# Kernel optimization log

Measured on AMD Instinct MI355X. Metric: run time of the kernel, lower is better.

The kernel has to match this reference:

```python
import jax, jax.numpy as jnp
import numpy as np
import math

D_MODEL = 1024
N_HEADS = 16
HEAD_DIM = 64


def setup_inputs() -> dict:
    key = jax.random.key(0)
    k_x, k_q, k_k, k_v, k_o = jax.random.split(key, 5)
    lecun = jax.nn.initializers.lecun_normal()
    return {
        "x": jax.random.normal(k_x, (4, 2048, D_MODEL), dtype=jnp.float32),
        "W_q": lecun(k_q, (N_HEADS, D_MODEL, HEAD_DIM), jnp.float32),
        "W_k": lecun(k_k, (N_HEADS, D_MODEL, HEAD_DIM), jnp.float32),
        "W_v": lecun(k_v, (N_HEADS, D_MODEL, HEAD_DIM), jnp.float32),
        "W_o": lecun(k_o, (D_MODEL, D_MODEL), jnp.float32),
    }


def reference(x, W_q, W_k, W_v, W_o):
    # x: [b, l, e]; W_{q,k,v}: [h, e, d]; W_o: [e, e]
    q = jnp.einsum('ble,hed->bhld', x, W_q)
    k = jnp.einsum('ble,hed->bhld', x, W_k)
    v = jnp.einsum('ble,hed->bhld', x, W_v)
    scores = jnp.einsum('bhld,bhsd->bhls', q, k) / math.sqrt(HEAD_DIM)
    attn = jax.nn.softmax(scores, axis=-1)
    av = jnp.einsum('bhls,bhsd->bhld', attn, v)  # [b, h, l, d]
    b, h, l, d = av.shape
    concat = jnp.transpose(av, (0, 2, 1, 3)).reshape(b, l, h * d)
    out = jnp.einsum('ble,eo->blo', concat, W_o)
    return jnp.asarray(out, dtype=jnp.float32)
```

## Files before the change

kernel.cpp:

```cpp
#include <hip/hip_runtime.h>

#define BATCH 4
#define LSEQ  2048
#define DM    1024
#define NH    16
#define HD    64
#define NTOK  (BATCH * LSEQ)

typedef _Float16 f16x8 __attribute__((ext_vector_type(8)));
typedef _Float16 f16x4 __attribute__((ext_vector_type(4)));
typedef __fp16   hf16x2 __attribute__((ext_vector_type(2)));
typedef float    f32x4 __attribute__((ext_vector_type(4)));

typedef __attribute__((address_space(1))) const unsigned int GU32;
typedef __attribute__((address_space(3))) unsigned int LU32;

__device__ __forceinline__ void gload_lds16(const _Float16* g, _Float16* l)
{
    __builtin_amdgcn_global_load_lds(
        (GU32*)(unsigned long long)g,
        (LU32*)(unsigned int)(unsigned long long)l, 16, 0, 0);
}


__global__ __launch_bounds__(256) void cvt_kernel(const float* __restrict__ src,
                                                  _Float16* __restrict__ dst, int n4)
{
    int i = blockIdx.x * 256 + threadIdx.x;
    if (i >= n4) return;
    float4 v = ((const float4*)src)[i];
    f16x4 h;
    h[0] = (_Float16)v.x; h[1] = (_Float16)v.y; h[2] = (_Float16)v.z; h[3] = (_Float16)v.w;
    ((f16x4*)dst)[i] = h;
}

__global__ __launch_bounds__(256) void tconv_kernel(const float* __restrict__ src,
                                                    _Float16* __restrict__ dst, int E, int D)
{
    const int d0 = blockIdx.x * 64, e0 = blockIdx.y * 64;
    const size_t mo = (size_t)blockIdx.z * E * D;
    src += mo; dst += mo;
    __shared__ float Ls[64][65];
    const int t = threadIdx.x;
    #pragma unroll
    for (int j = 0; j < 4; ++j) {
        int cidx = t + j * 256;
        int row = cidx >> 4, col4 = (cidx & 15) * 4;
        float4 v = *(const float4*)&src[(size_t)(e0 + row) * D + d0 + col4];
        Ls[row][col4] = v.x; Ls[row][col4+1] = v.y; Ls[row][col4+2] = v.z; Ls[row][col4+3] = v.w;
    }
    __syncthreads();
    const int dd = t & 63, sc = t >> 6;
    alignas(16) _Float16 tmp[16];
    #pragma unroll
    for (int i = 0; i < 16; ++i) tmp[i] = (_Float16)Ls[sc * 16 + i][dd];
    *(f16x8*)&dst[(size_t)(d0 + dd) * E + e0 + sc * 16]     = *(f16x8*)&tmp[0];
    *(f16x8*)&dst[(size_t)(d0 + dd) * E + e0 + sc * 16 + 8] = *(f16x8*)&tmp[8];
}

__global__ __launch_bounds__(256) void tv_kernel(const _Float16* __restrict__ v,
                                                 _Float16* __restrict__ vt)
{
    const int l0 = blockIdx.x * 64;
    const int bh = blockIdx.y;
    __shared__ _Float16 Ls[64][72];
    const int t = threadIdx.x;
    #pragma unroll
    for (int j = 0; j < 2; ++j) {
        int cidx = t + j * 256;
        int row = cidx >> 3, col8 = (cidx & 7) * 8;
        *(f16x8*)&Ls[row][col8] = *(const f16x8*)&v[((size_t)bh * LSEQ + l0 + row) * HD + col8];
    }
    __syncthreads();
    const int dd = t & 63, sc = t >> 6;
    alignas(16) _Float16 tmp[16];
    #pragma unroll
    for (int i = 0; i < 16; ++i) tmp[i] = Ls[sc * 16 + i][dd];
    *(f16x8*)&vt[((size_t)bh * HD + dd) * LSEQ + l0 + sc * 16]     = *(f16x8*)&tmp[0];
    *(f16x8*)&vt[((size_t)bh * HD + dd) * LSEQ + l0 + sc * 16 + 8] = *(f16x8*)&tmp[8];
}

template<int MODE>
__global__ __launch_bounds__(256) void gemm_kernel(
    const _Float16* __restrict__ A, const _Float16* __restrict__ B,
    float* __restrict__ out32,
    _Float16* __restrict__ qo, _Float16* __restrict__ ko, _Float16* __restrict__ vo)
{
    const int n0 = blockIdx.x * 128, m0 = blockIdx.y * 128;
    __shared__ _Float16 As[128 * 64];
    __shared__ _Float16 Bs[128 * 64];
    const int t = threadIdx.x;
    const int lane = t & 63, w = t >> 6;
    const int quad = lane >> 4, c = lane & 15;
    const int wm = (w & 1) * 64, wn = (w >> 1) * 64;
    const int srow = lane >> 3;
    const int scol8 = ((lane & 7) ^ (lane >> 3)) * 8;

    const int colsw = (quad ^ (c & 7)) * 8;
    const _Float16* Ap0 = &As[(wm + c) * 64 + colsw];
    const _Float16* Ap1 = &As[(wm + c) * 64 + (colsw ^ 32)];
    const _Float16* Bp0 = &Bs[(wn + c) * 64 + colsw];
    const _Float16* Bp1 = &Bs[(wn + c) * 64 + (colsw ^ 32)];

    f32x4 acc[4][4];
    #pragma unroll
    for (int i = 0; i < 4; ++i)
        #pragma unroll
        for (int j = 0; j < 4; ++j) acc[i][j] = {0.f, 0.f, 0.f, 0.f};

    for (int e0 = 0; e0 < DM; e0 += 64) {
        __syncthreads();
        #pragma unroll
        for (int j = 0; j < 4; ++j) {
            int ch = w * 4 + j;
            gload_lds16(A + (size_t)(m0 + ch * 8 + srow) * DM + e0 + scol8, As + ch * 512);
            gload_lds16(B + (size_t)(n0 + ch * 8 + srow) * DM + e0 + scol8, Bs + ch * 512);
        }
        __syncthreads();
        #pragma unroll
        for (int kc = 0; kc < 2; ++kc) {
            const _Float16* Ap = kc ? Ap1 : Ap0;
            const _Float16* Bp = kc ? Bp1 : Bp0;
            f16x8 af[4], bf[4];
            #pragma unroll
            for (int mt = 0; mt < 4; ++mt) af[mt] = *(const f16x8*)(Ap + mt * 1024);
            #pragma unroll
            for (int nt = 0; nt < 4; ++nt) bf[nt] = *(const f16x8*)(Bp + nt * 1024);
            #pragma unroll
            for (int mt = 0; mt < 4; ++mt)
                #pragma unroll
                for (int nt = 0; nt < 4; ++nt)
                    acc[mt][nt] = __builtin_amdgcn_mfma_f32_16x16x32_f16(af[mt], bf[nt], acc[mt][nt], 0, 0, 0);
        }
    }

    if (MODE == 0) {
        #pragma unroll
        for (int mt = 0; mt < 4; ++mt)
            #pragma unroll
            for (int nt = 0; nt < 4; ++nt)
                #pragma unroll
                for (int r = 0; r < 4; ++r) {
                    int row = m0 + wm + mt * 16 + quad * 4 + r;
                    int col = n0 + wn + nt * 16 + c;
                    out32[(size_t)row * DM + col] = acc[mt][nt][r];
                }
    } else {
        const int mi = (n0 + wn) >> 6;
        const int which = mi >> 4, hh = mi & 15;
        _Float16* dst = (which == 0) ? qo : (which == 1) ? ko : vo;
        const float vs = (which == 0) ? 0.18033688011112042f : 1.0f;
        #pragma unroll
        for (int mt = 0; mt < 4; ++mt)
            #pragma unroll
            for (int nt = 0; nt < 4; ++nt)
                #pragma unroll
                for (int r = 0; r < 4; ++r) {
                    int tok = m0 + wm + mt * 16 + quad * 4 + r;
                    int b = tok >> 11, l = tok & (LSEQ - 1);
                    int d = nt * 16 + c;
                    dst[((size_t)(b * NH + hh) * LSEQ + l) * HD + d] = (_Float16)(acc[mt][nt][r] * vs);
                }
    }
}

__global__ __launch_bounds__(128, 2) void attn_kernel(
    const _Float16* __restrict__ Qg, const _Float16* __restrict__ Kg,
    const _Float16* __restrict__ Vtg, _Float16* __restrict__ concat)
{
    const int bh = blockIdx.x;
    const int q0 = blockIdx.y * 128;
    const int b = bh >> 4, h = bh & (NH - 1);
    __shared__ _Float16 Ks[64 * 64];
    __shared__ _Float16 Vts[64 * 64];
    __shared__ _Float16 Ps[2][64][72];
    const int t = threadIdx.x;
    const int lane = t & 63, w = t >> 6;
    const int quad = lane >> 4, c = lane & 15;
    const int srow = lane >> 3;
    const int scol8 = ((lane & 7) ^ (lane >> 3)) * 8;

    const int colsw = (quad ^ (c & 7)) * 8;
    const _Float16* Kp0 = &Ks[c * 64 + colsw];
    const _Float16* Kp1 = &Ks[c * 64 + (colsw ^ 32)];
    const _Float16* Vp0 = &Vts[c * 64 + colsw];
    const _Float16* Vp1 = &Vts[c * 64 + (colsw ^ 32)];
    _Float16*       PsW = &Ps[w][c][quad * 4];
    const _Float16* PsR = &Ps[w][c][quad * 8];

    f16x8 qf[4][2];
    #pragma unroll
    for (int mi = 0; mi < 4; ++mi)
        #pragma unroll
        for (int kc = 0; kc < 2; ++kc)
            qf[mi][kc] = *(const f16x8*)&Qg[((size_t)bh * LSEQ + q0 + w * 64 + mi * 16 + c) * HD + kc * 32 + quad * 8];

    f32x4 o[4][4];
    #pragma unroll
    for (int mi = 0; mi < 4; ++mi)
        #pragma unroll
        for (int dt = 0; dt < 4; ++dt) o[mi][dt] = {0.f, 0.f, 0.f, 0.f};
    float lp[4] = {0.f, 0.f, 0.f, 0.f};

    for (int s0 = 0; s0 < LSEQ; s0 += 64) {
        __syncthreads();
        #pragma unroll
        for (int j = 0; j < 4; ++j) {
            int ch = w * 4 + j;
            gload_lds16(Kg  + ((size_t)bh * LSEQ + s0 + ch * 8 + srow) * HD + scol8, Ks  + ch * 512);
            gload_lds16(Vtg + ((size_t)bh * HD + ch * 8 + srow) * LSEQ + s0 + scol8, Vts + ch * 512);
        }
        __syncthreads();

        #pragma unroll
        for (int st = 0; st < 4; ++st) {
            f32x4 sT[4];
            #pragma unroll
            for (int mi = 0; mi < 4; ++mi) sT[mi] = {0.f, 0.f, 0.f, 0.f};
            #pragma unroll
            for (int kc = 0; kc < 2; ++kc) {
                f16x8 kf = *(const f16x8*)((kc ? Kp1 : Kp0) + st * 1024);
                #pragma unroll
                for (int mi = 0; mi < 4; ++mi)
                    sT[mi] = __builtin_amdgcn_mfma_f32_16x16x32_f16(kf, qf[mi][kc], sT[mi], 0, 0, 0);
            }
            #pragma unroll
            for (int mi = 0; mi < 4; ++mi) {
                float p0 = __builtin_amdgcn_exp2f(sT[mi][0]);
                float p1 = __builtin_amdgcn_exp2f(sT[mi][1]);
                float p2 = __builtin_amdgcn_exp2f(sT[mi][2]);
                float p3 = __builtin_amdgcn_exp2f(sT[mi][3]);
                lp[mi] += (p0 + p1) + (p2 + p3);
                union { hf16x2 h2[2]; f16x4 h4; } u;
                u.h2[0] = __builtin_amdgcn_cvt_pkrtz(p0, p1);
                u.h2[1] = __builtin_amdgcn_cvt_pkrtz(p2, p3);
                *(f16x4*)(PsW + mi * 1152 + st * 16) = u.h4;
            }
        }

        #pragma unroll
        for (int sc = 0; sc < 2; ++sc) {
            f16x8 pf[4];
            #pragma unroll
            for (int mi = 0; mi < 4; ++mi)
                pf[mi] = *(const f16x8*)(PsR + mi * 1152 + sc * 32);
            #pragma unroll
            for (int dt = 0; dt < 4; ++dt) {
                f16x8 vf = *(const f16x8*)((sc ? Vp1 : Vp0) + dt * 1024);
                #pragma unroll
                for (int mi = 0; mi < 4; ++mi)
                    o[mi][dt] = __builtin_amdgcn_mfma_f32_16x16x32_f16(pf[mi], vf, o[mi][dt], 0, 0, 0);
            }
        }
    }

    #pragma unroll
    for (int mi = 0; mi < 4; ++mi) {
        lp[mi] += __shfl_xor(lp[mi], 16);
        lp[mi] += __shfl_xor(lp[mi], 32);
    }

    #pragma unroll
    for (int mi = 0; mi < 4; ++mi)
        #pragma unroll
        for (int r = 0; r < 4; ++r) {
            float inv = 1.f / __shfl(lp[mi], quad * 4 + r);
            int row = q0 + w * 64 + mi * 16 + quad * 4 + r;
            #pragma unroll
            for (int dt = 0; dt < 4; ++dt)
                concat[((size_t)b * LSEQ + row) * DM + h * HD + dt * 16 + c] =
                    (_Float16)(o[mi][dt][r] * inv);
        }
}

extern "C" void kernel_launch(void* const* d_in, const int* in_sizes, int n_in,
                              void* d_out, int out_size, void* d_ws, size_t ws_size,
                              hipStream_t stream)
{
    (void)in_sizes; (void)n_in; (void)out_size; (void)ws_size;

    const float* x  = (const float*)d_in[0];
    const float* Wq = (const float*)d_in[1];
    const float* Wk = (const float*)d_in[2];
    const float* Wv = (const float*)d_in[3];
    const float* Wo = (const float*)d_in[4];
    float* out = (float*)d_out;

    const size_t XE = (size_t)NTOK * DM;
    const size_t WQKV = (size_t)3 * NH * HD * DM;
    _Float16* xh  = (_Float16*)d_ws;
    _Float16* WtA = xh + XE;
    _Float16* Wot = WtA + WQKV;
    _Float16* q   = Wot + (size_t)DM * DM;
    _Float16* k   = q + XE;
    _Float16* v   = k + XE;
    _Float16* vt  = v + XE;
    _Float16* cc  = vt + XE;

    cvt_kernel<<<8192, 256, 0, stream>>>(x, xh, (int)(XE / 4));
    tconv_kernel<<<dim3(1, 16, 16), 256, 0, stream>>>(Wq, WtA,                    DM, HD);
    tconv_kernel<<<dim3(1, 16, 16), 256, 0, stream>>>(Wk, WtA + NH * HD * DM,     DM, HD);
    tconv_kernel<<<dim3(1, 16, 16), 256, 0, stream>>>(Wv, WtA + 2 * NH * HD * DM, DM, HD);
    tconv_kernel<<<dim3(16, 16, 1), 256, 0, stream>>>(Wo, Wot, DM, DM);

    gemm_kernel<1><<<dim3(24, 64), 256, 0, stream>>>(xh, WtA, nullptr, q, k, v);
    tv_kernel<<<dim3(LSEQ / 64, 64), 256, 0, stream>>>(v, vt);
    attn_kernel<<<dim3(64, LSEQ / 128), 128, 0, stream>>>(q, k, vt, cc);
    gemm_kernel<0><<<dim3(8, 64), 256, 0, stream>>>(cc, Wot, out, nullptr, nullptr, nullptr);
}
```

Measured before the change: 290.4 us.

## Double-buffer K/V tiles in attention, fuse V transpose into QKV GEMM epilogue

The attention kernel now double-buffers its K and V^T tiles in LDS. The next tile is issued via global_load_lds before computing on the current one, which leaves one barrier per iteration instead of two and overlaps load latency with MFMA work. The QKV GEMM epilogue writes V directly in transposed [b,h,d,l] layout with packed 4-element stores, so the separate tv_kernel pass and its intermediate buffer are gone. The three Q/K/V weight conversion launches are merged into one tconv3 launch. The costs are double the K/V LDS, which may lower occupancy, and possibly less coalesced V stores.

After: 312.3 us. 7.5% more time.

```diff
diff --git a/kernel.cpp b/kernel.cpp
--- a/kernel.cpp
+++ b/kernel.cpp
@@ -34,12 +34,38 @@
     ((f16x4*)dst)[i] = h;
 }
 
+__global__ __launch_bounds__(256) void tconv3_kernel(
+    const float* __restrict__ Wq, const float* __restrict__ Wk,
+    const float* __restrict__ Wv, _Float16* __restrict__ dst)
+{
+    const int z = blockIdx.z;
+    const int which = z >> 4, h = z & 15;
+    const float* __restrict__ src =
+        ((which == 0) ? Wq : (which == 1) ? Wk : Wv) + (size_t)h * DM * HD;
+    _Float16* __restrict__ d = dst + (size_t)z * DM * HD;
+    const int e0 = blockIdx.y * 64;
+    __shared__ float Ls[64][65];
+    const int t = threadIdx.x;
+    #pragma unroll
+    for (int j = 0; j < 4; ++j) {
+        int cidx = t + j * 256;
+        int row = cidx >> 4, col4 = (cidx & 15) * 4;
+        float4 v = *(const float4*)&src[(size_t)(e0 + row) * HD + col4];
+        Ls[row][col4] = v.x; Ls[row][col4+1] = v.y; Ls[row][col4+2] = v.z; Ls[row][col4+3] = v.w;
+    }
+    __syncthreads();
+    const int dd = t & 63, sc = t >> 6;
+    alignas(16) _Float16 tmp[16];
+    #pragma unroll
+    for (int i = 0; i < 16; ++i) tmp[i] = (_Float16)Ls[sc * 16 + i][dd];
+    *(f16x8*)&d[(size_t)dd * DM + e0 + sc * 16]     = *(f16x8*)&tmp[0];
+    *(f16x8*)&d[(size_t)dd * DM + e0 + sc * 16 + 8] = *(f16x8*)&tmp[8];
+}
+
 __global__ __launch_bounds__(256) void tconv_kernel(const float* __restrict__ src,
                                                     _Float16* __restrict__ dst, int E, int D)
 {
     const int d0 = blockIdx.x * 64, e0 = blockIdx.y * 64;
-    const size_t mo = (size_t)blockIdx.z * E * D;
-    src += mo; dst += mo;
     __shared__ float Ls[64][65];
     const int t = threadIdx.x;
     #pragma unroll
@@ -58,33 +84,11 @@
     *(f16x8*)&dst[(size_t)(d0 + dd) * E + e0 + sc * 16 + 8] = *(f16x8*)&tmp[8];
 }
 
-__global__ __launch_bounds__(256) void tv_kernel(const _Float16* __restrict__ v,
-                                                 _Float16* __restrict__ vt)
-{
-    const int l0 = blockIdx.x * 64;
-    const int bh = blockIdx.y;
-    __shared__ _Float16 Ls[64][72];
-    const int t = threadIdx.x;
-    #pragma unroll
-    for (int j = 0; j < 2; ++j) {
-        int cidx = t + j * 256;
-        int row = cidx >> 3, col8 = (cidx & 7) * 8;
-        *(f16x8*)&Ls[row][col8] = *(const f16x8*)&v[((size_t)bh * LSEQ + l0 + row) * HD + col8];
-    }
-    __syncthreads();
-    const int dd = t & 63, sc = t >> 6;
-    alignas(16) _Float16 tmp[16];
-    #pragma unroll
-    for (int i = 0; i < 16; ++i) tmp[i] = Ls[sc * 16 + i][dd];
-    *(f16x8*)&vt[((size_t)bh * HD + dd) * LSEQ + l0 + sc * 16]     = *(f16x8*)&tmp[0];
-    *(f16x8*)&vt[((size_t)bh * HD + dd) * LSEQ + l0 + sc * 16 + 8] = *(f16x8*)&tmp[8];
-}
-
 template<int MODE>
 __global__ __launch_bounds__(256) void gemm_kernel(
     const _Float16* __restrict__ A, const _Float16* __restrict__ B,
     float* __restrict__ out32,
-    _Float16* __restrict__ qo, _Float16* __restrict__ ko, _Float16* __restrict__ vo)
+    _Float16* __restrict__ qo, _Float16* __restrict__ ko, _Float16* __restrict__ vto)
 {
     const int n0 = blockIdx.x * 128, m0 = blockIdx.y * 128;
     __shared__ _Float16 As[128 * 64];
@@ -148,19 +152,37 @@
     } else {
         const int mi = (n0 + wn) >> 6;
         const int which = mi >> 4, hh = mi & 15;
-        _Float16* dst = (which == 0) ? qo : (which == 1) ? ko : vo;
-        const float vs = (which == 0) ? 0.18033688011112042f : 1.0f;
-        #pragma unroll
-        for (int mt = 0; mt < 4; ++mt)
-            #pragma unroll
-            for (int nt = 0; nt < 4; ++nt)
-                #pragma unroll
-                for (int r = 0; r < 4; ++r) {
-                    int tok = m0 + wm + mt * 16 + quad * 4 + r;
-                    int b = tok >> 11, l = tok & (LSEQ - 1);
+        if (which == 2) {
+            #pragma unroll
+            for (int mt = 0; mt < 4; ++mt) {
+                int tok0 = m0 + wm + mt * 16 + quad * 4;
+                int b = tok0 >> 11, l = tok0 & (LSEQ - 1);
+                #pragma unroll
+                for (int nt = 0; nt < 4; ++nt) {
                     int d = nt * 16 + c;
-                    dst[((size_t)(b * NH + hh) * LSEQ + l) * HD + d] = (_Float16)(acc[mt][nt][r] * vs);
+                    f16x4 pk;
+                    pk[0] = (_Float16)acc[mt][nt][0];
+                    pk[1] = (_Float16)acc[mt][nt][1];
+                    pk[2] = (_Float16)acc[mt][nt][2];
+                    pk[3] = (_Float16)acc[mt][nt][3];
+                    *(f16x4*)&vto[((size_t)(b * NH + hh) * HD + d) * LSEQ + l] = pk;
                 }
+            }
+        } else {
+            _Float16* dst = (which == 0) ? qo : ko;
+            const float vs = (which == 0) ? 0.18033688011112042f : 1.0f;
+            #pragma unroll
+            for (int mt = 0; mt < 4; ++mt)
+                #pragma unroll
+                for (int nt = 0; nt < 4; ++nt)
+                    #pragma unroll
+                    for (int r = 0; r < 4; ++r) {
+                        int tok = m0 + wm + mt * 16 + quad * 4 + r;
+                        int b = tok >> 11, l = tok & (LSEQ - 1);
+                        int d = nt * 16 + c;
+                        dst[((size_t)(b * NH + hh) * LSEQ + l) * HD + d] = (_Float16)(acc[mt][nt][r] * vs);
+                    }
+        }
     }
 }
 
@@ -171,8 +193,8 @@
     const int bh = blockIdx.x;
     const int q0 = blockIdx.y * 128;
     const int b = bh >> 4, h = bh & (NH - 1);
-    __shared__ _Float16 Ks[64 * 64];
-    __shared__ _Float16 Vts[64 * 64];
+    __shared__ _Float16 Ks[2][64 * 64];
+    __shared__ _Float16 Vts[2][64 * 64];
     __shared__ _Float16 Ps[2][64][72];
     const int t = threadIdx.x;
     const int lane = t & 63, w = t >> 6;
@@ -181,13 +203,14 @@
     const int scol8 = ((lane & 7) ^ (lane >> 3)) * 8;
 
     const int colsw = (quad ^ (c & 7)) * 8;
-    const _Float16* Kp0 = &Ks[c * 64 + colsw];
-    const _Float16* Kp1 = &Ks[c * 64 + (colsw ^ 32)];
-    const _Float16* Vp0 = &Vts[c * 64 + colsw];
-    const _Float16* Vp1 = &Vts[c * 64 + (colsw ^ 32)];
+    const int fb0 = c * 64 + colsw;
+    const int fb1 = c * 64 + (colsw ^ 32);
     _Float16*       PsW = &Ps[w][c][quad * 4];
     const _Float16* PsR = &Ps[w][c][quad * 8];
 
+    const _Float16* Kgb = Kg  + (size_t)bh * LSEQ * HD;
+    const _Float16* Vgb = Vtg + (size_t)bh * HD * LSEQ;
+
     f16x8 qf[4][2];
     #pragma unroll
     for (int mi = 0; mi < 4; ++mi)
@@ -202,15 +225,30 @@
         for (int dt = 0; dt < 4; ++dt) o[mi][dt] = {0.f, 0.f, 0.f, 0.f};
     float lp[4] = {0.f, 0.f, 0.f, 0.f};
 
-    for (int s0 = 0; s0 < LSEQ; s0 += 64) {
-        __syncthreads();
-        #pragma unroll
-        for (int j = 0; j < 4; ++j) {
-            int ch = w * 4 + j;
-            gload_lds16(Kg  + ((size_t)bh * LSEQ + s0 + ch * 8 + srow) * HD + scol8, Ks  + ch * 512);
-            gload_lds16(Vtg + ((size_t)bh * HD + ch * 8 + srow) * LSEQ + s0 + scol8, Vts + ch * 512);
-        }
-        __syncthreads();
+    #pragma unroll
+    for (int j = 0; j < 4; ++j) {
+        int ch = w * 4 + j;
+        gload_lds16(Kgb + (size_t)(ch * 8 + srow) * HD + scol8,        &Ks[0][ch * 512]);
+        gload_lds16(Vgb + (size_t)(ch * 8 + srow) * LSEQ + 0 + scol8,  &Vts[0][ch * 512]);
+    }
+    __syncthreads();
+
+    for (int it = 0; it < LSEQ / 64; ++it) {
+        const int buf = it & 1;
+        if (it + 1 < LSEQ / 64) {
+            int s1 = (it + 1) * 64;
+            #pragma unroll
+            for (int j = 0; j < 4; ++j) {
+                int ch = w * 4 + j;
+                gload_lds16(Kgb + (size_t)(s1 + ch * 8 + srow) * HD + scol8,  &Ks[buf ^ 1][ch * 512]);
+                gload_lds16(Vgb + (size_t)(ch * 8 + srow) * LSEQ + s1 + scol8, &Vts[buf ^ 1][ch * 512]);
+            }
+        }
+
+        const _Float16* K0 = &Ks[buf][fb0];
+        const _Float16* K1 = &Ks[buf][fb1];
+        const _Float16* V0 = &Vts[buf][fb0];
+        const _Float16* V1 = &Vts[buf][fb1];
 
         #pragma unroll
         for (int st = 0; st < 4; ++st) {
@@ -219,7 +257,7 @@
             for (int mi = 0; mi < 4; ++mi) sT[mi] = {0.f, 0.f, 0.f, 0.f};
             #pragma unroll
             for (int kc = 0; kc < 2; ++kc) {
-                f16x8 kf = *(const f16x8*)((kc ? Kp1 : Kp0) + st * 1024);
+                f16x8 kf = *(const f16x8*)((kc ? K1 : K0) + st * 1024);
                 #pragma unroll
                 for (int mi = 0; mi < 4; ++mi)
                     sT[mi] = __builtin_amdgcn_mfma_f32_16x16x32_f16(kf, qf[mi][kc], sT[mi], 0, 0, 0);
@@ -246,12 +284,14 @@
                 pf[mi] = *(const f16x8*)(PsR + mi * 1152 + sc * 32);
             #pragma unroll
             for (int dt = 0; dt < 4; ++dt) {
-                f16x8 vf = *(const f16x8*)((sc ? Vp1 : Vp0) + dt * 1024);
+                f16x8 vf = *(const f16x8*)((sc ? V1 : V0) + dt * 1024);
                 #pragma unroll
                 for (int mi = 0; mi < 4; ++mi)
                     o[mi][dt] = __builtin_amdgcn_mfma_f32_16x16x32_f16(pf[mi], vf, o[mi][dt], 0, 0, 0);
             }
         }
+
+        __syncthreads();
     }
 
     #pragma unroll
@@ -293,18 +333,14 @@
     _Float16* Wot = WtA + WQKV;
     _Float16* q   = Wot + (size_t)DM * DM;
     _Float16* k   = q + XE;
-    _Float16* v   = k + XE;
-    _Float16* vt  = v + XE;
+    _Float16* vt  = k + XE;
     _Float16* cc  = vt + XE;
 
     cvt_kernel<<<8192, 256, 0, stream>>>(x, xh, (int)(XE / 4));
-    tconv_kernel<<<dim3(1, 16, 16), 256, 0, stream>>>(Wq, WtA,                    DM, HD);
-    tconv_kernel<<<dim3(1, 16, 16), 256, 0, stream>>>(Wk, WtA + NH * HD * DM,     DM, HD);
-    tconv_kernel<<<dim3(1, 16, 16), 256, 0, stream>>>(Wv, WtA + 2 * NH * HD * DM, DM, HD);
+    tconv3_kernel<<<dim3(1, 16, 48), 256, 0, stream>>>(Wq, Wk, Wv, WtA);
     tconv_kernel<<<dim3(16, 16, 1), 256, 0, stream>>>(Wo, Wot, DM, DM);
 
-    gemm_kernel<1><<<dim3(24, 64), 256, 0, stream>>>(xh, WtA, nullptr, q, k, v);
-    tv_kernel<<<dim3(LSEQ / 64, 64), 256, 0, stream>>>(v, vt);
+    gemm_kernel<1><<<dim3(24, 64), 256, 0, stream>>>(xh, WtA, nullptr, q, k, vt);
     attn_kernel<<<dim3(64, LSEQ / 128), 128, 0, stream>>>(q, k, vt, cc);
     gemm_kernel<0><<<dim3(8, 64), 256, 0, stream>>>(cc, Wot, out, nullptr, nullptr, nullptr);
 }
```
